# Performance work log

Measured on AMD Instinct MI355X. Metric: run time of the kernel, lower is better.

Reference implementation:

```python
import jax, jax.numpy as jnp
import numpy as np

B, C, W = 8, 128, 4096
REDUCTION = 8
D = C // REDUCTION  # 16


def setup_inputs() -> dict:
    key = jax.random.key(0)
    ks = jax.random.split(key, 7)
    scale = 0.05
    return {
        "x": jax.random.normal(ks[0], (B, C, W), dtype=jnp.float32),
        "Wq": jax.random.normal(ks[1], (D, C), dtype=jnp.float32) * scale,
        "bq": jax.random.normal(ks[2], (D,), dtype=jnp.float32) * scale,
        "Wk": jax.random.normal(ks[3], (D, C), dtype=jnp.float32) * scale,
        "bk": jax.random.normal(ks[4], (D,), dtype=jnp.float32) * scale,
        "Wv": jax.random.normal(ks[5], (C, C), dtype=jnp.float32) * scale,
        "bv": jax.random.normal(ks[6], (C,), dtype=jnp.float32) * scale,
    }


def reference(x, Wq, bq, Wk, bk, Wv, bv):
    # 1x1 Conv1d == per-position linear over channel axis
    q = jnp.einsum('dc,bcw->bdw', Wq, x) + bq[None, :, None]   # [B, D, W]
    k = jnp.einsum('dc,bcw->bdw', Wk, x) + bk[None, :, None]   # [B, D, W]
    v = jnp.einsum('oc,bcw->bow', Wv, x) + bv[None, :, None]   # [B, C, W]
    scale = D ** (-0.5)
    # scores[b,i,j] = q[b,:,i] . k[b,:,j]
    scores = jnp.einsum('bdi,bdj->bij', q, k) * scale          # [B, W, W]
    attn = jax.nn.softmax(scores, axis=-1)
    # torch.bmm(value, attn): context[b,c,w] = sum_j v[b,c,j] * attn[b,j,w]
    context = jnp.einsum('bcj,bjw->bcw', v, attn)              # [B, C, W]
    return context + x
```

## Files before the change

kernel.cpp:

```cpp
#include <hip/hip_runtime.h>

#define B_ 8
#define C_ 128
#define W_ 4096
#define D_ 16
#define SCALE2 0.3606737602222409f

typedef short bf16x8 __attribute__((ext_vector_type(8)));
typedef float f32x4 __attribute__((ext_vector_type(4)));
typedef float f32x16 __attribute__((ext_vector_type(16)));

__device__ __forceinline__ unsigned short f2bf(float f) {
    unsigned int u = __float_as_uint(f);
    u += 0x7fffu + ((u >> 16) & 1u);
    return (unsigned short)(u >> 16);
}
__device__ __forceinline__ float bf2f(unsigned short h) {
    return __uint_as_float(((unsigned int)h) << 16);
}
__device__ __forceinline__ unsigned int pk2bf(float lo, float hi) {
    return __builtin_amdgcn_perm(__float_as_uint(hi), __float_as_uint(lo), 0x07060302u);
}
__device__ __forceinline__ bf16x8 uint4_as_bf8(uint4 u) {
    union { uint4 u; bf16x8 v; } t;
    t.u = u;
    return t.v;
}
__device__ __forceinline__ uint4 exp2s(f32x16 s, int r0, float4 ra, float4 rb) {
    return make_uint4(
        pk2bf(__builtin_amdgcn_exp2f(s[r0+0]-ra.x), __builtin_amdgcn_exp2f(s[r0+1]-ra.y)),
        pk2bf(__builtin_amdgcn_exp2f(s[r0+2]-ra.z), __builtin_amdgcn_exp2f(s[r0+3]-ra.w)),
        pk2bf(__builtin_amdgcn_exp2f(s[r0+4]-rb.x), __builtin_amdgcn_exp2f(s[r0+5]-rb.y)),
        pk2bf(__builtin_amdgcn_exp2f(s[r0+6]-rb.z), __builtin_amdgcn_exp2f(s[r0+7]-rb.w)));
}
__device__ __forceinline__ int xswz(int j, int c8) {
    return c8 ^ (j & 7) ^ ((j >> 3) & 7);
}

__global__ __launch_bounds__(256) void prep(
    const float* __restrict__ Wq, const float* __restrict__ Wk, const float* __restrict__ Wv,
    unsigned short* __restrict__ Wvbf, unsigned short* __restrict__ Wqkbf)
{
    int g = blockIdx.x * 256 + threadIdx.x;
    const float* src; unsigned short* dst; float sc = 1.0f;
    if (g < 4096)      { src = Wv + g * 4;            dst = Wvbf + g * 4; }
    else if (g < 4608) { int t = g - 4096; src = Wq + t * 4; dst = Wqkbf + t * 4; sc = SCALE2; }
    else               { int t = g - 4608; src = Wk + t * 4; dst = Wqkbf + 2048 + t * 4; }
    float4 v = *(const float4*)src;
    unsigned short h[4] = {f2bf(v.x * sc), f2bf(v.y * sc), f2bf(v.z * sc), f2bf(v.w * sc)};
    *(ushort4*)dst = *(ushort4*)h;
}

__global__ __launch_bounds__(256) void proj(
    const float* __restrict__ x, const unsigned short* __restrict__ Wvbf,
    const unsigned short* __restrict__ Wqkbf,
    const float* __restrict__ bqp, const float* __restrict__ bkp, const float* __restrict__ bvp,
    unsigned short* __restrict__ qws2, unsigned short* __restrict__ kws2,
    unsigned short* __restrict__ vws2)
{
    __shared__ unsigned short xbf[32 * 128];
    __shared__ unsigned short outs[128 * 36];
    __shared__ unsigned short qk_s[2][32][24];

    int b  = blockIdx.x & 7;
    int j0 = (blockIdx.x >> 3) * 32;
    int jt = j0 >> 5;
    int tid = threadIdx.x;
    int wid = tid >> 6, lane = tid & 63, n = lane & 15, q4 = lane >> 4;

    {
        unsigned int* xbf32 = (unsigned int*)xbf;
#pragma unroll
        for (int i = 0; i < 8; i++) {
            int p = tid + 256 * i;
            int c2 = p >> 5;
            int j  = p & 31;
            const float* xp = x + (size_t)(b * C_ + 2 * c2) * W_ + j0 + j;
            float lo = xp[0];
            float hi = xp[W_];
            xbf32[j * 64 + xswz(j, c2 >> 2) * 4 + (c2 & 3)] = pk2bf(lo, hi);
        }
    }
    __syncthreads();

    const f32x4 zero = {0.f, 0.f, 0.f, 0.f};
    f32x4 accv[2][2]; f32x4 accqk = zero;
#pragma unroll
    for (int os = 0; os < 2; os++)
#pragma unroll
        for (int js = 0; js < 2; js++) accv[os][js] = zero;

    int isK = wid >> 1;
    int jsm = wid & 1;

#pragma unroll
    for (int kk = 0; kk < 128; kk += 32) {
        bf16x8 av[2], aqkf, bx[2];
#pragma unroll
        for (int os = 0; os < 2; os++)
            av[os] = *(const bf16x8*)(Wvbf + (wid * 32 + os * 16 + n) * 128 + kk + q4 * 8);
        aqkf = *(const bf16x8*)(Wqkbf + (isK * 16 + n) * 128 + kk + q4 * 8);
#pragma unroll
        for (int js = 0; js < 2; js++) {
            int j = js * 16 + n;
            bx[js] = *(const bf16x8*)&xbf[j * 128 + xswz(j, (kk >> 3) + q4) * 8];
        }
#pragma unroll
        for (int os = 0; os < 2; os++)
#pragma unroll
            for (int js = 0; js < 2; js++)
                accv[os][js] = __builtin_amdgcn_mfma_f32_16x16x32_bf16(av[os], bx[js], accv[os][js], 0, 0, 0);
        accqk = __builtin_amdgcn_mfma_f32_16x16x32_bf16(aqkf, bx[jsm], accqk, 0, 0, 0);
    }

    {
        int pos = jsm * 16 + n;
        const float* bias = isK ? bkp : bqp;
        float bsc = isK ? 1.0f : SCALE2;
#pragma unroll
        for (int r = 0; r < 4; r++)
            qk_s[isK][pos][q4 * 4 + r] = f2bf(accqk[r] + bias[q4 * 4 + r] * bsc);
    }

    float bvv[2][4];
#pragma unroll
    for (int os = 0; os < 2; os++)
#pragma unroll
        for (int r = 0; r < 4; r++) bvv[os][r] = bvp[wid * 32 + os * 16 + q4 * 4 + r];
#pragma unroll
    for (int os = 0; os < 2; os++)
#pragma unroll
        for (int js = 0; js < 2; js++)
#pragma unroll
            for (int r = 0; r < 4; r++) {
                int c = wid * 32 + os * 16 + q4 * 4 + r;
                int j = js * 16 + n;
                outs[c * 36 + j] = f2bf(accv[os][js][r] + bvv[os][r]);
            }
    __syncthreads();

    if (tid < 128) {
        int qk = tid >> 6, hh = (tid >> 5) & 1, jl = tid & 31;
        uint4 v = *(const uint4*)&qk_s[qk][jl][hh * 8];
        unsigned short* dst = (qk ? kws2 : qws2)
            + (size_t)(b * 128 + jt) * 512 + hh * 256 + jl * 8;
        *(uint4*)dst = v;
    }
#pragma unroll
    for (int rep = 0; rep < 2; rep++) {
        int t = tid + rep * 256;
        int c = t & 127, sel = t >> 7;
        int jb = (sel >> 1) * 16 + (sel & 1) * 4;
        uint2 lo = *(const uint2*)&outs[c * 36 + jb];
        uint2 hi = *(const uint2*)&outs[c * 36 + jb + 8];
        *(uint4*)(vws2 + ((size_t)(b * 128 + jt) * 4 + sel) * 1024 + c * 8) =
            make_uint4(lo.x, lo.y, hi.x, hi.y);
    }
}

__global__ __launch_bounds__(256) void row_stats(
    const unsigned short* __restrict__ qws2, const unsigned short* __restrict__ kws2,
    float* __restrict__ rlp)
{
    int blk = blockIdx.x;
    int b = blk & 7;
    int j0 = ((blk >> 3) & 31) * 128;
    int wsp = blk >> 8;
    int tid = threadIdx.x;
    int wid = tid >> 6, lane = tid & 63, wl = lane & 31, h = lane >> 5;

    const unsigned short* qb = qws2 + (size_t)b * 65536;
    const unsigned short* kb = kws2 + (size_t)b * 65536;
    int jt = (j0 >> 5) + wid;

    bf16x8 aq = *(const bf16x8*)(qb + (size_t)jt * 512 + h * 256 + wl * 8);
    f32x16 zero16 = {0.f,0.f,0.f,0.f,0.f,0.f,0.f,0.f,0.f,0.f,0.f,0.f,0.f,0.f,0.f,0.f};

    float lt[16];
#pragma unroll
    for (int r = 0; r < 16; r++) lt[r] = 0.f;

    bf16x8 bkc = *(const bf16x8*)(kb + (size_t)(wsp * 32) * 512 + h * 256 + wl * 8);
    for (int t = 0; t < 32; t++) {
        f32x16 s = __builtin_amdgcn_mfma_f32_32x32x16_bf16(aq, bkc, zero16, 0, 0, 0);
        int tn = wsp * 32 + ((t + 1) & 31);
        bkc = *(const bf16x8*)(kb + (size_t)tn * 512 + h * 256 + wl * 8);
#pragma unroll
        for (int r = 0; r < 16; r++) lt[r] += __builtin_amdgcn_exp2f(s[r]);
    }
#pragma unroll
    for (int mask = 1; mask < 32; mask <<= 1)
#pragma unroll
        for (int r = 0; r < 16; r++) lt[r] += __shfl_xor(lt[r], mask, 64);
    if (wl == 0) {
#pragma unroll
        for (int g = 0; g < 4; g++) {
            f32x4 v = {lt[4*g+0], lt[4*g+1], lt[4*g+2], lt[4*g+3]};
            *(f32x4*)(rlp + (size_t)wsp * 32768 + (size_t)b * W_ + j0 + wid * 32 + 4 * h + 8 * g) = v;
        }
    }
}

__global__ __launch_bounds__(256) void rfin(const float* __restrict__ rlp,
                                            float* __restrict__ rlog)
{
    int g = blockIdx.x * 256 + threadIdx.x;
    float l = rlp[g] + rlp[32768 + g] + rlp[65536 + g] + rlp[98304 + g];
    rlog[g] = __builtin_amdgcn_logf(l);
}

__global__ __launch_bounds__(512, 4) void attn_out(
    const float* __restrict__ x, const unsigned short* __restrict__ qws2,
    const unsigned short* __restrict__ kws2, const unsigned short* __restrict__ vws2,
    const float* __restrict__ rlog, float* __restrict__ out)
{
    __shared__ uint4 p_lds[2][1024];
    __shared__ float red[128 * 68];

    int b  = blockIdx.x & 7;
    int w0 = (blockIdx.x >> 3) * 64;
    int tid = threadIdx.x;
    int wid = tid >> 6, lane = tid & 63, wl = lane & 31, h = lane >> 5;
    int cq = wid >> 1, kh = wid & 1;

    const unsigned short* qb  = qws2 + (size_t)b * 65536;
    const unsigned short* kb  = kws2 + (size_t)b * 65536;
    const uint4* vtb4 = (const uint4*)(vws2 + (size_t)b * 524288) + h * 128 + (cq * 32 + wl);
    const float* rlb = rlog + (size_t)b * W_;
    const int qoff = h * 256 + wl * 8;

    bf16x8 bk = *(const bf16x8*)(kb + (size_t)((w0 >> 5) + kh) * 512 + h * 256 + wl * 8);

    f32x16 zero16 = {0.f,0.f,0.f,0.f,0.f,0.f,0.f,0.f,0.f,0.f,0.f,0.f,0.f,0.f,0.f,0.f};
    f32x16 acc[2];
    acc[0] = zero16; acc[1] = zero16;

    const int wbase = cq * 256 + h * 64 + kh * 32 + wl;
    const int rbase = kh * 512 + h * 64 + wl;

    bf16x8 aq = *(const bf16x8*)(qb + (size_t)cq * 512 + qoff);
    uint4 vfA[4], vfB[4];
#pragma unroll
    for (int kf = 0; kf < 4; kf++)
        vfA[kf] = vtb4[(size_t)(kh * 4 + kf) * 256];
    {
        int jb0 = cq * 32 + 4 * h;
        float4 rl0 = *(const float4*)(rlb + jb0);
        float4 rl1 = *(const float4*)(rlb + jb0 + 8);
        float4 rl2 = *(const float4*)(rlb + jb0 + 16);
        float4 rl3 = *(const float4*)(rlb + jb0 + 24);
        f32x16 s = __builtin_amdgcn_mfma_f32_32x32x16_bf16(aq, bk, zero16, 0, 0, 0);
        aq = *(const bf16x8*)(qb + (size_t)(4 + cq) * 512 + qoff);
        p_lds[0][wbase]       = exp2s(s, 0, rl0, rl1);
        p_lds[0][wbase + 128] = exp2s(s, 8, rl2, rl3);
    }
    __syncthreads();

#define STEP(IT, CUR, VC, VN)                                                        \
    {                                                                                \
        const int it_ = (IT);                                                        \
        int kgb = ((it_ + 1) & 31) * 8 + kh * 4;                                     \
        _Pragma("unroll") for (int kf = 0; kf < 4; kf++)                             \
            VN[kf] = vtb4[(size_t)(kgb + kf) * 256];                                 \
        int jbn = ((it_ + 1) & 31) * 128 + cq * 32 + 4 * h;                          \
        float4 rl0 = *(const float4*)(rlb + jbn);                                    \
        float4 rl1 = *(const float4*)(rlb + jbn + 8);                                \
        float4 rl2 = *(const float4*)(rlb + jbn + 16);                               \
        float4 rl3 = *(const float4*)(rlb + jbn + 24);                               \
        f32x16 s = __builtin_amdgcn_mfma_f32_32x32x16_bf16(aq, bk, zero16, 0, 0, 0); \
        aq = *(const bf16x8*)(qb + (size_t)(((it_ + 2) & 31) * 4 + cq) * 512 + qoff);\
        __builtin_amdgcn_s_setprio(1);                                               \
        _Pragma("unroll") for (int kf = 0; kf < 4; kf++) {                           \
            bf16x8 af = uint4_as_bf8(VC[kf]);                                        \
            _Pragma("unroll") for (int nt = 0; nt < 2; nt++) {                       \
                bf16x8 bp = uint4_as_bf8(p_lds[CUR][rbase + kf * 128 + nt * 32]);    \
                acc[nt] = __builtin_amdgcn_mfma_f32_32x32x16_bf16(af, bp, acc[nt], 0, 0, 0); \
            }                                                                        \
        }                                                                            \
        __builtin_amdgcn_s_setprio(0);                                               \
        p_lds[(CUR) ^ 1][wbase]       = exp2s(s, 0, rl0, rl1);                       \
        p_lds[(CUR) ^ 1][wbase + 128] = exp2s(s, 8, rl2, rl3);                       \
        __syncthreads();                                                             \
    }

    for (int i2 = 0; i2 < 16; i2++) {
        STEP(2 * i2,     0, vfA, vfB);
        STEP(2 * i2 + 1, 1, vfB, vfA);
    }
#undef STEP

#define CROW(r) (cq * 32 + ((r) & 3) + 8 * ((r) >> 2) + 4 * h)
    if (kh == 1) {
#pragma unroll
        for (int nt = 0; nt < 2; nt++)
#pragma unroll
            for (int r = 0; r < 16; r++)
                red[CROW(r) * 68 + nt * 32 + wl] = acc[nt][r];
    }
    __syncthreads();
    if (kh == 0) {
#pragma unroll
        for (int nt = 0; nt < 2; nt++)
#pragma unroll
            for (int r = 0; r < 16; r++) {
                int o = CROW(r) * 68 + nt * 32 + wl;
                red[o] += acc[nt][r];
            }
    }
#undef CROW
    __syncthreads();

#pragma unroll
    for (int u = 0; u < 4; u++) {
        int k = tid + 512 * u;
        int c = k >> 4, wseg = (k & 15) * 4;
        size_t gidx = (size_t)(b * C_ + c) * W_ + w0 + wseg;
        float4 xv = *(const float4*)(x + gidx);
        const float* sp = &red[c * 68 + wseg];
        *(float4*)(out + gidx) = make_float4(sp[0] + xv.x, sp[1] + xv.y, sp[2] + xv.z, sp[3] + xv.w);
    }
}

extern "C" void kernel_launch(void* const* d_in, const int* in_sizes, int n_in,
                              void* d_out, int out_size, void* d_ws, size_t ws_size,
                              hipStream_t stream)
{
    const float* x  = (const float*)d_in[0];
    const float* Wq = (const float*)d_in[1];
    const float* bq = (const float*)d_in[2];
    const float* Wk = (const float*)d_in[3];
    const float* bk = (const float*)d_in[4];
    const float* Wv = (const float*)d_in[5];
    const float* bv = (const float*)d_in[6];
    float* out = (float*)d_out;

    unsigned short* qws2 = (unsigned short*)d_ws;
    unsigned short* kws2 = qws2 + (size_t)524288;
    unsigned short* vws2 = kws2 + (size_t)524288;
    unsigned short* Wvbf = vws2 + (size_t)4194304;
    unsigned short* Wqkbf = Wvbf + 16384;
    float* rlp = (float*)(Wqkbf + 4096);
    float* rlg = rlp + 131072;

    prep<<<20, 256, 0, stream>>>(Wq, Wk, Wv, Wvbf, Wqkbf);
    proj<<<1024, 256, 0, stream>>>(x, Wvbf, Wqkbf, bq, bk, bv, qws2, kws2, vws2);
    row_stats<<<1024, 256, 0, stream>>>(qws2, kws2, rlp);
    rfin<<<128, 256, 0, stream>>>(rlp, rlg);
    attn_out<<<512, 512, 0, stream>>>(x, qws2, kws2, vws2, rlg, out);
}
```

Before: 163.1 us.

## Fold softmax row normalizer into V and convert weights inside proj

Moves the softmax normalization out of the attention inner loop. Instead of subtracting log row-sums before exp2 for every score, a new vscale kernel multiplies the bf16 V workspace by 1/rowsum for each key position, so attn_out only computes the plain exp2. The separate weight-prep kernel is also removed: proj now loads the fp32 weights and converts them to bf16 inline. This cuts launches and per-iteration loads of row statistics, but adds a read-modify-write pass over V and an extra bf16 rounding. Because no max is subtracted before exp2, unnormalized exponentials could overflow or lose precision.

```diff
diff --git a/kernel.cpp b/kernel.cpp
--- a/kernel.cpp
+++ b/kernel.cpp
@@ -26,34 +26,27 @@
     t.u = u;
     return t.v;
 }
-__device__ __forceinline__ uint4 exp2s(f32x16 s, int r0, float4 ra, float4 rb) {
+__device__ __forceinline__ bf16x8 ld8w(const float* p, float sc) {
+    float4 lo = *(const float4*)p, hi = *(const float4*)(p + 4);
+    union { uint4 u; bf16x8 v; } t;
+    t.u = make_uint4(pk2bf(lo.x * sc, lo.y * sc), pk2bf(lo.z * sc, lo.w * sc),
+                     pk2bf(hi.x * sc, hi.y * sc), pk2bf(hi.z * sc, hi.w * sc));
+    return t.v;
+}
+__device__ __forceinline__ uint4 exp2pkq(f32x16 s, int r0) {
     return make_uint4(
-        pk2bf(__builtin_amdgcn_exp2f(s[r0+0]-ra.x), __builtin_amdgcn_exp2f(s[r0+1]-ra.y)),
-        pk2bf(__builtin_amdgcn_exp2f(s[r0+2]-ra.z), __builtin_amdgcn_exp2f(s[r0+3]-ra.w)),
-        pk2bf(__builtin_amdgcn_exp2f(s[r0+4]-rb.x), __builtin_amdgcn_exp2f(s[r0+5]-rb.y)),
-        pk2bf(__builtin_amdgcn_exp2f(s[r0+6]-rb.z), __builtin_amdgcn_exp2f(s[r0+7]-rb.w)));
+        pk2bf(__builtin_amdgcn_exp2f(s[r0+0]), __builtin_amdgcn_exp2f(s[r0+1])),
+        pk2bf(__builtin_amdgcn_exp2f(s[r0+2]), __builtin_amdgcn_exp2f(s[r0+3])),
+        pk2bf(__builtin_amdgcn_exp2f(s[r0+4]), __builtin_amdgcn_exp2f(s[r0+5])),
+        pk2bf(__builtin_amdgcn_exp2f(s[r0+6]), __builtin_amdgcn_exp2f(s[r0+7])));
 }
 __device__ __forceinline__ int xswz(int j, int c8) {
     return c8 ^ (j & 7) ^ ((j >> 3) & 7);
 }
 
-__global__ __launch_bounds__(256) void prep(
+__global__ __launch_bounds__(256) void proj(
+    const float* __restrict__ x,
     const float* __restrict__ Wq, const float* __restrict__ Wk, const float* __restrict__ Wv,
-    unsigned short* __restrict__ Wvbf, unsigned short* __restrict__ Wqkbf)
-{
-    int g = blockIdx.x * 256 + threadIdx.x;
-    const float* src; unsigned short* dst; float sc = 1.0f;
-    if (g < 4096)      { src = Wv + g * 4;            dst = Wvbf + g * 4; }
-    else if (g < 4608) { int t = g - 4096; src = Wq + t * 4; dst = Wqkbf + t * 4; sc = SCALE2; }
-    else               { int t = g - 4608; src = Wk + t * 4; dst = Wqkbf + 2048 + t * 4; }
-    float4 v = *(const float4*)src;
-    unsigned short h[4] = {f2bf(v.x * sc), f2bf(v.y * sc), f2bf(v.z * sc), f2bf(v.w * sc)};
-    *(ushort4*)dst = *(ushort4*)h;
-}
-
-__global__ __launch_bounds__(256) void proj(
-    const float* __restrict__ x, const unsigned short* __restrict__ Wvbf,
-    const unsigned short* __restrict__ Wqkbf,
     const float* __restrict__ bqp, const float* __restrict__ bkp, const float* __restrict__ bvp,
     unsigned short* __restrict__ qws2, unsigned short* __restrict__ kws2,
     unsigned short* __restrict__ vws2)
@@ -92,14 +85,16 @@
 
     int isK = wid >> 1;
     int jsm = wid & 1;
+    const float* wqk = isK ? Wk : Wq;
+    const float qksc = isK ? 1.0f : SCALE2;
 
 #pragma unroll
     for (int kk = 0; kk < 128; kk += 32) {
         bf16x8 av[2], aqkf, bx[2];
 #pragma unroll
         for (int os = 0; os < 2; os++)
-            av[os] = *(const bf16x8*)(Wvbf + (wid * 32 + os * 16 + n) * 128 + kk + q4 * 8);
-        aqkf = *(const bf16x8*)(Wqkbf + (isK * 16 + n) * 128 + kk + q4 * 8);
+            av[os] = ld8w(Wv + (size_t)(wid * 32 + os * 16 + n) * 128 + kk + q4 * 8, 1.0f);
+        aqkf = ld8w(wqk + (size_t)n * 128 + kk + q4 * 8, qksc);
 #pragma unroll
         for (int js = 0; js < 2; js++) {
             int j = js * 16 + n;
@@ -201,18 +196,41 @@
     }
 }
 
-__global__ __launch_bounds__(256) void rfin(const float* __restrict__ rlp,
-                                            float* __restrict__ rlog)
-{
-    int g = blockIdx.x * 256 + threadIdx.x;
-    float l = rlp[g] + rlp[32768 + g] + rlp[65536 + g] + rlp[98304 + g];
-    rlog[g] = __builtin_amdgcn_logf(l);
+__global__ __launch_bounds__(256) void vscale(unsigned short* __restrict__ vws2,
+                                              const float* __restrict__ rlp)
+{
+    __shared__ float rl[16];
+    int bi = blockIdx.x;
+    int g0 = bi * 256;
+    int kf = (g0 >> 8) & 1, jt = (g0 >> 9) & 127, b = g0 >> 16;
+    int tid = threadIdx.x;
+    if (tid < 16) {
+        int idx = b * W_ + jt * 32 + kf * 16 + tid;
+        float l = rlp[idx] + rlp[32768 + idx] + rlp[65536 + idx] + rlp[98304 + idx];
+        rl[tid] = 1.0f / l;
+    }
+    __syncthreads();
+
+    int g = g0 + tid;
+    int hh = (g >> 7) & 1;
+    float4 r0 = *(const float4*)&rl[4 * hh];
+    float4 r1 = *(const float4*)&rl[4 * hh + 8];
+    uint4 v = *(const uint4*)(vws2 + (size_t)g * 8);
+    unsigned int o0 = pk2bf(bf2f((unsigned short)(v.x & 0xffffu)) * r0.x,
+                            bf2f((unsigned short)(v.x >> 16))     * r0.y);
+    unsigned int o1 = pk2bf(bf2f((unsigned short)(v.y & 0xffffu)) * r0.z,
+                            bf2f((unsigned short)(v.y >> 16))     * r0.w);
+    unsigned int o2 = pk2bf(bf2f((unsigned short)(v.z & 0xffffu)) * r1.x,
+                            bf2f((unsigned short)(v.z >> 16))     * r1.y);
+    unsigned int o3 = pk2bf(bf2f((unsigned short)(v.w & 0xffffu)) * r1.z,
+                            bf2f((unsigned short)(v.w >> 16))     * r1.w);
+    *(uint4*)(vws2 + (size_t)g * 8) = make_uint4(o0, o1, o2, o3);
 }
 
 __global__ __launch_bounds__(512, 4) void attn_out(
     const float* __restrict__ x, const unsigned short* __restrict__ qws2,
     const unsigned short* __restrict__ kws2, const unsigned short* __restrict__ vws2,
-    const float* __restrict__ rlog, float* __restrict__ out)
+    float* __restrict__ out)
 {
     __shared__ uint4 p_lds[2][1024];
     __shared__ float red[128 * 68];
@@ -226,7 +244,6 @@
     const unsigned short* qb  = qws2 + (size_t)b * 65536;
     const unsigned short* kb  = kws2 + (size_t)b * 65536;
     const uint4* vtb4 = (const uint4*)(vws2 + (size_t)b * 524288) + h * 128 + (cq * 32 + wl);
-    const float* rlb = rlog + (size_t)b * W_;
     const int qoff = h * 256 + wl * 8;
 
     bf16x8 bk = *(const bf16x8*)(kb + (size_t)((w0 >> 5) + kh) * 512 + h * 256 + wl * 8);
@@ -244,15 +261,10 @@
     for (int kf = 0; kf < 4; kf++)
         vfA[kf] = vtb4[(size_t)(kh * 4 + kf) * 256];
     {
-        int jb0 = cq * 32 + 4 * h;
-        float4 rl0 = *(const float4*)(rlb + jb0);
-        float4 rl1 = *(const float4*)(rlb + jb0 + 8);
-        float4 rl2 = *(const float4*)(rlb + jb0 + 16);
-        float4 rl3 = *(const float4*)(rlb + jb0 + 24);
         f32x16 s = __builtin_amdgcn_mfma_f32_32x32x16_bf16(aq, bk, zero16, 0, 0, 0);
         aq = *(const bf16x8*)(qb + (size_t)(4 + cq) * 512 + qoff);
-        p_lds[0][wbase]       = exp2s(s, 0, rl0, rl1);
-        p_lds[0][wbase + 128] = exp2s(s, 8, rl2, rl3);
+        p_lds[0][wbase]       = exp2pkq(s, 0);
+        p_lds[0][wbase + 128] = exp2pkq(s, 8);
     }
     __syncthreads();
 
@@ -262,11 +274,6 @@
         int kgb = ((it_ + 1) & 31) * 8 + kh * 4;                                     \
         _Pragma("unroll") for (int kf = 0; kf < 4; kf++)                             \
             VN[kf] = vtb4[(size_t)(kgb + kf) * 256];                                 \
-        int jbn = ((it_ + 1) & 31) * 128 + cq * 32 + 4 * h;                          \
-        float4 rl0 = *(const float4*)(rlb + jbn);                                    \
-        float4 rl1 = *(const float4*)(rlb + jbn + 8);                                \
-        float4 rl2 = *(const float4*)(rlb + jbn + 16);                               \
-        float4 rl3 = *(const float4*)(rlb + jbn + 24);                               \
         f32x16 s = __builtin_amdgcn_mfma_f32_32x32x16_bf16(aq, bk, zero16, 0, 0, 0); \
         aq = *(const bf16x8*)(qb + (size_t)(((it_ + 2) & 31) * 4 + cq) * 512 + qoff);\
         __builtin_amdgcn_s_setprio(1);                                               \
@@ -278,8 +285,8 @@
             }                                                                        \
         }                                                                            \
         __builtin_amdgcn_s_setprio(0);                                               \
-        p_lds[(CUR) ^ 1][wbase]       = exp2s(s, 0, rl0, rl1);                       \
-        p_lds[(CUR) ^ 1][wbase + 128] = exp2s(s, 8, rl2, rl3);                       \
+        p_lds[(CUR) ^ 1][wbase]       = exp2pkq(s, 0);                               \
+        p_lds[(CUR) ^ 1][wbase + 128] = exp2pkq(s, 8);                               \
         __syncthreads();                                                             \
     }
 
@@ -337,14 +344,10 @@
     unsigned short* qws2 = (unsigned short*)d_ws;
     unsigned short* kws2 = qws2 + (size_t)524288;
     unsigned short* vws2 = kws2 + (size_t)524288;
-    unsigned short* Wvbf = vws2 + (size_t)4194304;
-    unsigned short* Wqkbf = Wvbf + 16384;
-    float* rlp = (float*)(Wqkbf + 4096);
-    float* rlg = rlp + 131072;
-
-    prep<<<20, 256, 0, stream>>>(Wq, Wk, Wv, Wvbf, Wqkbf);
-    proj<<<1024, 256, 0, stream>>>(x, Wvbf, Wqkbf, bq, bk, bv, qws2, kws2, vws2);
+    float* rlp = (float*)(vws2 + (size_t)4194304);
+
+    proj<<<1024, 256, 0, stream>>>(x, Wq, Wk, Wv, bq, bk, bv, qws2, kws2, vws2);
     row_stats<<<1024, 256, 0, stream>>>(qws2, kws2, rlp);
-    rfin<<<128, 256, 0, stream>>>(rlp, rlg);
-    attn_out<<<512, 512, 0, stream>>>(x, qws2, kws2, vws2, rlg, out);
-}
+    vscale<<<2048, 256, 0, stream>>>(vws2, rlp);
+    attn_out<<<512, 512, 0, stream>>>(x, qws2, kws2, vws2, out);
+}
```

New measurement: 162.0 us. Within noise of the previous version (-0.7%).
